# Kernel tuning notes

Hardware: AMD Instinct MI355X
Metric: run time of the kernel (lower is better)

## Reference

```python
import jax, jax.numpy as jnp
import numpy as np

B = 8
N = 2048  # max_seqlen
H = 4
D = 64  # attention_dim
V = 64  # linear_dim
SEQ_LEN = 1024  # tokens per sequence
L = B * SEQ_LEN


def setup_inputs() -> dict:
    key = jax.random.key(0)
    kq, kk, kv, kc = jax.random.split(key, 4)
    tq = jax.random.normal(kq, (L, H * D), dtype=jnp.float32)
    tk = jax.random.normal(kk, (L, H * D), dtype=jnp.float32)
    tv = jax.random.normal(kv, (L, H * V), dtype=jnp.float32)
    offsets = (jnp.arange(B + 1, dtype=jnp.int64) * SEQ_LEN)
    num_candidates = jax.random.randint(kc, (B,), 1, 64, dtype=jnp.int32)
    return {
        "tq": tq, "tk": tk, "tv": tv,
        "offsets": offsets,
        "num_candidates": num_candidates,
        "max_seqlen": N,
        "num_contextuals": 8,
    }


def _valid_attn_mask(n, seq_lengths, num_targets, num_contextuals_vec, target_group_size=1):
    # Port of _get_valid_attn_mask (causal=True, max_attn_len=None, tensor contextuals).
    ids = jnp.arange(n)[None, :]                         # (1, N)
    max_ids = seq_lengths[:, None, None]                 # (B, 1, 1)
    ids = jnp.maximum(ids - num_contextuals_vec[:, None] + 1, 0)   # (B, N)
    max_ids = max_ids - num_contextuals_vec[:, None, None] + 1
    row = ids[:, :, None]                                # (B, N, N) row_ids
    col = ids[:, None, :]                                # col_ids
    dist = row - col
    valid = jnp.eye(n, dtype=bool)[None] | (dist > 0)    # causal
    # target-group mask
    tg = jnp.maximum(ids - max_ids[:, :, 0] + num_targets[:, None], -1) // target_group_size  # (B, N)
    tg_row = tg[:, :, None]
    tg_col = tg[:, None, :]
    tgm = (tg_row == tg_col) | (tg_row < 0) | (tg_col < 0)
    valid = valid & tgm
    max_ids = max_ids - num_targets[:, None, None]
    # contextual rows attend to everything before (adjusted) max_ids
    valid = valid | ((row == 0) & (col < max_ids))
    return valid


def reference(tq, tk, tv, offsets, num_candidates, max_seqlen, num_contextuals):
    n = max_seqlen
    alpha = 1.0 / (D ** 0.5)
    scaling = float(max_seqlen)  # scaling_seqlen == -1 -> max_seqlen
    l = tq.shape[0]
    b = offsets.shape[0] - 1

    q = tq.reshape(l, H, D)
    k = tk.reshape(l, H, D)
    v = tv.reshape(l, H, V)

    tok = jnp.arange(l)
    batch_idx = jnp.searchsorted(offsets, tok, side="right") - 1   # (L,)
    pos = tok - offsets[batch_idx]                                  # (L,)

    def pad(x):  # jagged -> (B, N, H, d)
        return jnp.zeros((b, n, H, x.shape[-1]), x.dtype).at[batch_idx, pos].set(x)

    pq, pk, pv = pad(q), pad(k), pad(v)

    scores = jnp.einsum("bxhd,byhd->bhxy", pq, pk) * alpha
    attn = jax.nn.silu(scores) / scaling

    seq_lengths = offsets[1:] - offsets[:-1]
    nc_vec = jnp.full((b,), num_contextuals, dtype=jnp.int32)
    mask = _valid_attn_mask(n, seq_lengths, num_candidates, nc_vec)
    attn = attn * mask[:, None].astype(attn.dtype)

    out = jnp.einsum("bhxy,byhv->bxhv", attn, pv)   # (B, N, H, V)
    jagged = out[batch_idx, pos]                     # (L, H, V)
    return jagged.reshape(l, H * V)
```

## Files before the change

kernel.cpp:

```cpp
#include <hip/hip_runtime.h>
#include <hip/hip_bf16.h>

typedef __attribute__((ext_vector_type(8))) short s16x8;
typedef __attribute__((ext_vector_type(4))) float f32x4;
typedef __attribute__((ext_vector_type(4))) unsigned short u16x4;
typedef __attribute__((ext_vector_type(4))) float fl4;

__device__ __forceinline__ unsigned short f2bf(float f) {
  union { __hip_bfloat16 b; unsigned short u; } cv;
  cv.b = __float2bfloat16(f);
  return cv.u;
}

__device__ __forceinline__ void gl_lds16(const void* g, void* l) {
  __builtin_amdgcn_global_load_lds(
      (const __attribute__((address_space(1))) unsigned int*)g,
      (__attribute__((address_space(3))) unsigned int*)l, 16, 0, 0);
}

__global__ __launch_bounds__(256)
void prep_all(const float* __restrict__ tq, const float* __restrict__ tk,
              const float* __restrict__ tv, unsigned short* __restrict__ ws)
{
  const int bid  = (int)blockIdx.x;
  const int role = bid >> 9;
  const int blk  = bid & 511;
  const int bh = blk >> 4, t = blk & 15;
  const int b = bh >> 2, h = bh & 3;
  const int tid = (int)threadIdx.x;
  unsigned short* dst = ws + (size_t)role * 2097152 + (size_t)blk * 4096;

  if (role < 2) {
    const int sy = tid >> 2, sq4 = tid & 3;
    const float* src = (role ? tq : tk) + ((size_t)(b*1024 + t*64 + sy))*256 + h*64;
    const float scale = role ? 0.125f : 1.0f;
    char* row = (char*)dst + sy*128;
    const int ssw = (sy & 7) << 4;
#pragma unroll
    for (int j2 = 0; j2 < 4; ++j2) {
      fl4 v = *(const fl4*)(src + (sq4 + 4*j2)*4);
      u16x4 p;
      p[0] = f2bf(v[0]*scale); p[1] = f2bf(v[1]*scale);
      p[2] = f2bf(v[2]*scale); p[3] = f2bf(v[3]*scale);
      *(u16x4*)(row + (((sq4 + 4*j2)*8) ^ ssw)) = p;
    }
  } else {
    const int vg = tid >> 6, vc = tid & 63;
    const float* src = tv + ((size_t)(b*1024 + t*64))*256 + h*64 + vc;
#pragma unroll
    for (int kp = 0; kp < 2; ++kp)
#pragma unroll
      for (int tu = 0; tu < 2; ++tu) {
        const int y0 = 32*kp + 16*tu + 4*vg;
        u16x4 p;
#pragma unroll
        for (int j2 = 0; j2 < 4; ++j2)
          p[j2] = f2bf(src[(size_t)(y0 + j2)*256] * 4.8828125e-4f);
        *(u16x4*)&dst[((kp*4 + vg)*64 + vc)*8 + 4*tu] = p;
      }
  }
}

__global__ __launch_bounds__(256)
void hstu_main(const unsigned short* __restrict__ Kb, const unsigned short* __restrict__ Qb,
               const unsigned short* __restrict__ Vb, const int* __restrict__ ncand,
               float* __restrict__ out)
{
  const int bid = (int)blockIdx.x;
  const int bh = bid & 31;
  const int jp = bid >> 5;
  const int qtile = (jp == 0) ? 0 : (jp == 8) ? 1 : (jp < 8 ? jp + 1 : 24 - jp);
  const int b = bh >> 2, h = bh & 3;
  const int tid = (int)threadIdx.x;
  const int w = tid >> 6, l = tid & 63;
  const int rl = l & 15, g = l >> 4;
  const int T = 1024 - ncand[b];
  const int qbase = qtile << 6;

  __shared__ unsigned short Qlds[4096];
  __shared__ unsigned short Klds[2][4096];
  __shared__ unsigned short Vlds[2][4096];

  const char* kt  = (const char*)(Kb + (size_t)bh * 16 * 4096);
  const char* vtb = (const char*)(Vb + (size_t)bh * 16 * 4096);

  {
    const char* qs = (const char*)(Qb + ((size_t)bh*16 + qtile)*4096) + w*2048 + l*16;
    char* qd = (char*)Qlds + w*2048;
    gl_lds16(qs, qd);
    gl_lds16(qs + 1024, qd + 1024);
  }

  auto stage = [&](int buf, int kv) {
    const char* ks = kt + (size_t)kv*8192 + w*2048 + l*16;
    char* kd = (char*)Klds[buf] + w*2048;
    gl_lds16(ks, kd); gl_lds16(ks + 1024, kd + 1024);
    const char* vs = vtb + (size_t)kv*8192 + w*2048 + l*16;
    char* vd = (char*)Vlds[buf] + w*2048;
    gl_lds16(vs, vd); gl_lds16(vs + 1024, vd + 1024);
  };

  stage(0, 0);
  __syncthreads();

  s16x8 qf0, qf1;
  {
    const int qr = w*16 + rl;
    const char* base = (const char*)Qlds + qr*128;
    const int sw = (qr & 7) << 4;
    qf0 = *(const s16x8*)(base + ((g*16) ^ sw));
    qf1 = *(const s16x8*)(base + ((64 + g*16) ^ sw));
  }

  f32x4 zero = {0.f, 0.f, 0.f, 0.f};
  f32x4 oacc[4];
#pragma unroll
  for (int i = 0; i < 4; ++i) oacc[i] = zero;

  const int rq = qbase + w*16 + rl;
  const int nkv = (qtile == 0) ? 16 : (qtile + 1);

  for (int t = 0; t < nkv; ++t) {
    const int cur = t & 1;
    if (t + 1 < nkv) stage(cur ^ 1, t + 1);

    if (qtile != 0 || t == 0 || w == 0) {
      f32x4 sacc[4];
#pragma unroll
      for (int i = 0; i < 4; ++i) sacc[i] = zero;
      const char* kb = (const char*)Klds[cur];
#pragma unroll
      for (int t4 = 0; t4 < 4; ++t4) {
        const int kr = t4*16 + rl;
        const char* base = kb + kr*128;
        const int sw = (kr & 7) << 4;
        s16x8 kf0 = *(const s16x8*)(base + ((g*16) ^ sw));
        s16x8 kf1 = *(const s16x8*)(base + ((64 + g*16) ^ sw));
        sacc[t4] = __builtin_amdgcn_mfma_f32_16x16x32_bf16(kf0, qf0, sacc[t4], 0, 0, 0);
        sacc[t4] = __builtin_amdgcn_mfma_f32_16x16x32_bf16(kf1, qf1, sacc[t4], 0, 0, 0);
      }
      s16x8 pa0, pa1;
#pragma unroll
      for (int t4 = 0; t4 < 4; ++t4) {
#pragma unroll
        for (int r = 0; r < 4; ++r) {
          const int y = t*64 + t4*16 + 4*g + r;
          const float s = sacc[t4][r];
          const float sig = __builtin_amdgcn_rcpf(1.f + __expf(-s));
          const bool valid = (rq < 8) ? (y < T)
                           : ((y <= rq) && ((rq < T) || (y < T) || (y == rq)));
          const float a = valid ? s * sig : 0.f;
          const short bv = (short)f2bf(a);
          if (t4 < 2) pa0[(t4 & 1)*4 + r] = bv;
          else        pa1[(t4 & 1)*4 + r] = bv;
        }
      }
      const unsigned short* vb = Vlds[cur];
#pragma unroll
      for (int vt = 0; vt < 4; ++vt) {
        const s16x8 vf0 = *(const s16x8*)&vb[((0*4 + g)*64 + vt*16 + rl)*8];
        oacc[vt] = __builtin_amdgcn_mfma_f32_16x16x32_bf16(pa0, vf0, oacc[vt], 0, 0, 0);
        const s16x8 vf1 = *(const s16x8*)&vb[((1*4 + g)*64 + vt*16 + rl)*8];
        oacc[vt] = __builtin_amdgcn_mfma_f32_16x16x32_bf16(pa1, vf1, oacc[vt], 0, 0, 0);
      }
    }
    __syncthreads();
  }

  float* dst = out + ((size_t)(b*1024 + qbase + w*16))*256 + h*64;
#pragma unroll
  for (int vt = 0; vt < 4; ++vt)
#pragma unroll
    for (int r = 0; r < 4; ++r)
      dst[(size_t)(4*g + r)*256 + vt*16 + rl] = oacc[vt][r];
}

extern "C" void kernel_launch(void* const* d_in, const int* in_sizes, int n_in,
                              void* d_out, int out_size, void* d_ws, size_t ws_size,
                              hipStream_t stream) {
  (void)in_sizes; (void)n_in; (void)out_size; (void)ws_size;
  const float* tq = (const float*)d_in[0];
  const float* tk = (const float*)d_in[1];
  const float* tv = (const float*)d_in[2];
  const int*   nc = (const int*)d_in[4];
  float* out = (float*)d_out;
  unsigned short* ws = (unsigned short*)d_ws;

  hipLaunchKernelGGL(prep_all, dim3(1536), dim3(256), 0, stream, tq, tk, tv, ws);
  const unsigned short* Kb = ws;
  const unsigned short* Qb = ws + 2097152;
  const unsigned short* Vb = ws + 4194304;
  hipLaunchKernelGGL(hstu_main, dim3(512), dim3(256), 0, stream, Kb, Qb, Vb, nc, out);
}
```

Measured before the change: 43.00 us.

## Use single-wave blocks reading K/V directly from global, fuse Q conversion

Restructures the main attention kernel so each 64-thread block handles one 16-row query group and reads K and V fragments straight from global memory, with no LDS staging, double buffering or block barriers. Q conversion to bf16 with scaling moves into the main kernel, which shrinks the prep kernel to K and V only. Blocks are ordered so the longest causal groups launch first, giving finer load balance across 2048 blocks. In exchange, K/V tiles are no longer shared across waves through LDS, so global and L2 traffic rises and load latency is no longer hidden by prefetch.

Result: slower. 47.61 us (+10.7%).

```diff
diff --git a/kernel.cpp b/kernel.cpp
--- a/kernel.cpp
+++ b/kernel.cpp
@@ -12,15 +12,9 @@
   return cv.u;
 }
 
-__device__ __forceinline__ void gl_lds16(const void* g, void* l) {
-  __builtin_amdgcn_global_load_lds(
-      (const __attribute__((address_space(1))) unsigned int*)g,
-      (__attribute__((address_space(3))) unsigned int*)l, 16, 0, 0);
-}
-
 __global__ __launch_bounds__(256)
-void prep_all(const float* __restrict__ tq, const float* __restrict__ tk,
-              const float* __restrict__ tv, unsigned short* __restrict__ ws)
+void prep_kv(const float* __restrict__ tk, const float* __restrict__ tv,
+             unsigned short* __restrict__ ws)
 {
   const int bid  = (int)blockIdx.x;
   const int role = bid >> 9;
@@ -30,19 +24,17 @@
   const int tid = (int)threadIdx.x;
   unsigned short* dst = ws + (size_t)role * 2097152 + (size_t)blk * 4096;
 
-  if (role < 2) {
+  if (role == 0) {
     const int sy = tid >> 2, sq4 = tid & 3;
-    const float* src = (role ? tq : tk) + ((size_t)(b*1024 + t*64 + sy))*256 + h*64;
-    const float scale = role ? 0.125f : 1.0f;
+    const float* src = tk + ((size_t)(b*1024 + t*64 + sy))*256 + h*64;
     char* row = (char*)dst + sy*128;
-    const int ssw = (sy & 7) << 4;
 #pragma unroll
     for (int j2 = 0; j2 < 4; ++j2) {
       fl4 v = *(const fl4*)(src + (sq4 + 4*j2)*4);
       u16x4 p;
-      p[0] = f2bf(v[0]*scale); p[1] = f2bf(v[1]*scale);
-      p[2] = f2bf(v[2]*scale); p[3] = f2bf(v[3]*scale);
-      *(u16x4*)(row + (((sq4 + 4*j2)*8) ^ ssw)) = p;
+      p[0] = f2bf(v[0]); p[1] = f2bf(v[1]);
+      p[2] = f2bf(v[2]); p[3] = f2bf(v[3]);
+      *(u16x4*)(row + (sq4 + 4*j2)*8) = p;
     }
   } else {
     const int vg = tid >> 6, vc = tid & 63;
@@ -61,118 +53,92 @@
   }
 }
 
-__global__ __launch_bounds__(256)
-void hstu_main(const unsigned short* __restrict__ Kb, const unsigned short* __restrict__ Qb,
-               const unsigned short* __restrict__ Vb, const int* __restrict__ ncand,
+__global__ __launch_bounds__(64)
+void hstu_main(const unsigned short* __restrict__ Kb, const unsigned short* __restrict__ Vb,
+               const float* __restrict__ tq, const int* __restrict__ ncand,
                float* __restrict__ out)
 {
   const int bid = (int)blockIdx.x;
   const int bh = bid & 31;
   const int jp = bid >> 5;
-  const int qtile = (jp == 0) ? 0 : (jp == 8) ? 1 : (jp < 8 ? jp + 1 : 24 - jp);
+  const int rg = (jp == 0) ? 0 : 64 - jp;
   const int b = bh >> 2, h = bh & 3;
-  const int tid = (int)threadIdx.x;
-  const int w = tid >> 6, l = tid & 63;
+  const int l = (int)threadIdx.x;
   const int rl = l & 15, g = l >> 4;
   const int T = 1024 - ncand[b];
-  const int qbase = qtile << 6;
-
-  __shared__ unsigned short Qlds[4096];
-  __shared__ unsigned short Klds[2][4096];
-  __shared__ unsigned short Vlds[2][4096];
-
-  const char* kt  = (const char*)(Kb + (size_t)bh * 16 * 4096);
-  const char* vtb = (const char*)(Vb + (size_t)bh * 16 * 4096);
-
-  {
-    const char* qs = (const char*)(Qb + ((size_t)bh*16 + qtile)*4096) + w*2048 + l*16;
-    char* qd = (char*)Qlds + w*2048;
-    gl_lds16(qs, qd);
-    gl_lds16(qs + 1024, qd + 1024);
-  }
-
-  auto stage = [&](int buf, int kv) {
-    const char* ks = kt + (size_t)kv*8192 + w*2048 + l*16;
-    char* kd = (char*)Klds[buf] + w*2048;
-    gl_lds16(ks, kd); gl_lds16(ks + 1024, kd + 1024);
-    const char* vs = vtb + (size_t)kv*8192 + w*2048 + l*16;
-    char* vd = (char*)Vlds[buf] + w*2048;
-    gl_lds16(vs, vd); gl_lds16(vs + 1024, vd + 1024);
-  };
-
-  stage(0, 0);
-  __syncthreads();
+  const int qr = rg << 4;
+  const int rq = qr + rl;
 
   s16x8 qf0, qf1;
   {
-    const int qr = w*16 + rl;
-    const char* base = (const char*)Qlds + qr*128;
-    const int sw = (qr & 7) << 4;
-    qf0 = *(const s16x8*)(base + ((g*16) ^ sw));
-    qf1 = *(const s16x8*)(base + ((64 + g*16) ^ sw));
+    const float* qs = tq + ((size_t)(b*1024 + rq))*256 + h*64 + g*8;
+    fl4 a = *(const fl4*)qs, b2 = *(const fl4*)(qs + 4);
+    fl4 c = *(const fl4*)(qs + 32), d2 = *(const fl4*)(qs + 36);
+#pragma unroll
+    for (int j = 0; j < 4; ++j) {
+      qf0[j]   = (short)f2bf(a[j]  * 0.125f);
+      qf0[j+4] = (short)f2bf(b2[j] * 0.125f);
+      qf1[j]   = (short)f2bf(c[j]  * 0.125f);
+      qf1[j+4] = (short)f2bf(d2[j] * 0.125f);
+    }
   }
+
+  const char* kt = (const char*)(Kb + (size_t)bh * 16 * 4096);
+  const char* vt = (const char*)(Vb + (size_t)bh * 16 * 4096);
 
   f32x4 zero = {0.f, 0.f, 0.f, 0.f};
   f32x4 oacc[4];
 #pragma unroll
   for (int i = 0; i < 4; ++i) oacc[i] = zero;
 
-  const int rq = qbase + w*16 + rl;
-  const int nkv = (qtile == 0) ? 16 : (qtile + 1);
+  const int nkv = (rg == 0) ? 16 : (rg >> 2) + 1;
 
   for (int t = 0; t < nkv; ++t) {
-    const int cur = t & 1;
-    if (t + 1 < nkv) stage(cur ^ 1, t + 1);
+    const char* kimg = kt + (size_t)t * 8192;
+    const char* vimg = vt + (size_t)t * 8192;
 
-    if (qtile != 0 || t == 0 || w == 0) {
-      f32x4 sacc[4];
+    f32x4 sacc[4];
 #pragma unroll
-      for (int i = 0; i < 4; ++i) sacc[i] = zero;
-      const char* kb = (const char*)Klds[cur];
+    for (int i = 0; i < 4; ++i) sacc[i] = zero;
 #pragma unroll
-      for (int t4 = 0; t4 < 4; ++t4) {
-        const int kr = t4*16 + rl;
-        const char* base = kb + kr*128;
-        const int sw = (kr & 7) << 4;
-        s16x8 kf0 = *(const s16x8*)(base + ((g*16) ^ sw));
-        s16x8 kf1 = *(const s16x8*)(base + ((64 + g*16) ^ sw));
-        sacc[t4] = __builtin_amdgcn_mfma_f32_16x16x32_bf16(kf0, qf0, sacc[t4], 0, 0, 0);
-        sacc[t4] = __builtin_amdgcn_mfma_f32_16x16x32_bf16(kf1, qf1, sacc[t4], 0, 0, 0);
-      }
-      s16x8 pa0, pa1;
+    for (int t4 = 0; t4 < 4; ++t4) {
+      const char* base = kimg + (t4*16 + rl)*128;
+      s16x8 kf0 = *(const s16x8*)(base + g*16);
+      s16x8 kf1 = *(const s16x8*)(base + 64 + g*16);
+      sacc[t4] = __builtin_amdgcn_mfma_f32_16x16x32_bf16(kf0, qf0, sacc[t4], 0, 0, 0);
+      sacc[t4] = __builtin_amdgcn_mfma_f32_16x16x32_bf16(kf1, qf1, sacc[t4], 0, 0, 0);
+    }
+    s16x8 pa0, pa1;
 #pragma unroll
-      for (int t4 = 0; t4 < 4; ++t4) {
+    for (int t4 = 0; t4 < 4; ++t4) {
 #pragma unroll
-        for (int r = 0; r < 4; ++r) {
-          const int y = t*64 + t4*16 + 4*g + r;
-          const float s = sacc[t4][r];
-          const float sig = __builtin_amdgcn_rcpf(1.f + __expf(-s));
-          const bool valid = (rq < 8) ? (y < T)
-                           : ((y <= rq) && ((rq < T) || (y < T) || (y == rq)));
-          const float a = valid ? s * sig : 0.f;
-          const short bv = (short)f2bf(a);
-          if (t4 < 2) pa0[(t4 & 1)*4 + r] = bv;
-          else        pa1[(t4 & 1)*4 + r] = bv;
-        }
-      }
-      const unsigned short* vb = Vlds[cur];
-#pragma unroll
-      for (int vt = 0; vt < 4; ++vt) {
-        const s16x8 vf0 = *(const s16x8*)&vb[((0*4 + g)*64 + vt*16 + rl)*8];
-        oacc[vt] = __builtin_amdgcn_mfma_f32_16x16x32_bf16(pa0, vf0, oacc[vt], 0, 0, 0);
-        const s16x8 vf1 = *(const s16x8*)&vb[((1*4 + g)*64 + vt*16 + rl)*8];
-        oacc[vt] = __builtin_amdgcn_mfma_f32_16x16x32_bf16(pa1, vf1, oacc[vt], 0, 0, 0);
+      for (int r = 0; r < 4; ++r) {
+        const int y = t*64 + t4*16 + 4*g + r;
+        const float s = sacc[t4][r];
+        const float sig = __builtin_amdgcn_rcpf(1.f + __expf(-s));
+        const bool valid = (rq < 8) ? (y < T)
+                         : ((y <= rq) && ((rq < T) || (y < T) || (y == rq)));
+        const float a = valid ? s * sig : 0.f;
+        const short bv = (short)f2bf(a);
+        if (t4 < 2) pa0[(t4 & 1)*4 + r] = bv;
+        else        pa1[(t4 & 1)*4 + r] = bv;
       }
     }
-    __syncthreads();
+#pragma unroll
+    for (int vti = 0; vti < 4; ++vti) {
+      const s16x8 vf0 = *(const s16x8*)(vimg + (((0*4 + g)*64 + vti*16 + rl)*8)*2);
+      oacc[vti] = __builtin_amdgcn_mfma_f32_16x16x32_bf16(pa0, vf0, oacc[vti], 0, 0, 0);
+      const s16x8 vf1 = *(const s16x8*)(vimg + (((1*4 + g)*64 + vti*16 + rl)*8)*2);
+      oacc[vti] = __builtin_amdgcn_mfma_f32_16x16x32_bf16(pa1, vf1, oacc[vti], 0, 0, 0);
+    }
   }
 
-  float* dst = out + ((size_t)(b*1024 + qbase + w*16))*256 + h*64;
+  float* dst = out + ((size_t)(b*1024 + qr))*256 + h*64;
 #pragma unroll
-  for (int vt = 0; vt < 4; ++vt)
+  for (int vti = 0; vti < 4; ++vti)
 #pragma unroll
     for (int r = 0; r < 4; ++r)
-      dst[(size_t)(4*g + r)*256 + vt*16 + rl] = oacc[vt][r];
+      dst[(size_t)(4*g + r)*256 + vti*16 + rl] = oacc[vti][r];
 }
 
 extern "C" void kernel_launch(void* const* d_in, const int* in_sizes, int n_in,
@@ -186,9 +152,8 @@
   float* out = (float*)d_out;
   unsigned short* ws = (unsigned short*)d_ws;
 
-  hipLaunchKernelGGL(prep_all, dim3(1536), dim3(256), 0, stream, tq, tk, tv, ws);
+  hipLaunchKernelGGL(prep_kv, dim3(1024), dim3(256), 0, stream, tk, tv, ws);
   const unsigned short* Kb = ws;
-  const unsigned short* Qb = ws + 2097152;
-  const unsigned short* Vb = ws + 4194304;
-  hipLaunchKernelGGL(hstu_main, dim3(512), dim3(256), 0, stream, Kb, Qb, Vb, nc, out);
+  const unsigned short* Vb = ws + 2097152;
+  hipLaunchKernelGGL(hstu_main, dim3(2048), dim3(64), 0, stream, Kb, Vb, tq, nc, out);
 }
```
